# Performance work log

Hardware: AMD Instinct MI355X
Metric: run time of the kernel (lower is better)

## Reference

```python
import jax, jax.numpy as jnp
import numpy as np

B, C, H, W = 96, 5, 256, 256
T, V = 256, 256          # indices.shape[0], indices.shape[1]
HEADS, DHEAD = 2, 156
E = HEADS * DHEAD        # 312
EPS = 1e-5


def setup_inputs() -> dict:
    key = jax.random.key(0)
    ks = jax.random.split(key, 16)
    # indices: a permutation of the HxW grid so each pixel is gathered/scattered exactly once,
    # channel 2 is a float scale applied at scatter time.
    rng = np.random.RandomState(0)
    perm = rng.permutation(H * W).reshape(T, V)
    rows = (perm // W).astype(np.float32)
    cols = (perm % W).astype(np.float32)
    scale = rng.rand(T, V).astype(np.float32)
    indices = jnp.asarray(np.stack([rows, cols, scale], axis=-1))  # [T, V, 3]

    s = 0.02
    inp = {
        "sino": jax.random.normal(ks[0], (B, C, H, W), jnp.float32),
        "indices": indices,
        "We": jax.random.normal(ks[1], (C * V, E), jnp.float32) * s,
        "be": jnp.zeros((E,), jnp.float32),
        "pos": jax.random.normal(ks[2], (1, T, E), jnp.float32),
        "Wq": jax.random.normal(ks[3], (E, E), jnp.float32) * s,
        "Wk": jax.random.normal(ks[4], (E, E), jnp.float32) * s,
        "Wv": jax.random.normal(ks[5], (E, E), jnp.float32) * s,
        "W1": jax.random.normal(ks[6], (E, E), jnp.float32) * s,
        "b1": jnp.zeros((E,), jnp.float32),
        "W2": jax.random.normal(ks[7], (E, E), jnp.float32) * s,
        "b2": jnp.zeros((E,), jnp.float32),
        "W3": jax.random.normal(ks[8], (E, E), jnp.float32) * s,
        "b3": jnp.zeros((E,), jnp.float32),
        "g_att": jnp.ones((E,), jnp.float32),
        "beta_att": jnp.zeros((E,), jnp.float32),
        "g_mlp": jnp.ones((E,), jnp.float32),
        "beta_mlp": jnp.zeros((E,), jnp.float32),
        "Wu": jax.random.normal(ks[9], (E, V), jnp.float32) * s,
        "bu": jnp.zeros((V,), jnp.float32),
    }
    return inp


def _ln(y, g, b):
    m = jnp.mean(y, axis=-1, keepdims=True)
    v = jnp.var(y, axis=-1, keepdims=True)
    return (y - m) * jax.lax.rsqrt(v + EPS) * g + b


def reference(sino, indices, We, be, pos, Wq, Wk, Wv, W1, b1, W2, b2, W3, b3,
              g_att, beta_att, g_mlp, beta_mlp, Wu, bu):
    r = indices[:, :, 0].astype(jnp.int32)   # [T, V]
    c = indices[:, :, 1].astype(jnp.int32)   # [T, V]
    sc = indices[:, :, 2]                    # [T, V]

    # gather: sino[:, :, r, c] -> [B, C, T, V]
    x = sino[:, :, r, c]
    # 'bd c t v -> bd t (c v)'
    xt = jnp.transpose(x, (0, 2, 1, 3)).reshape(x.shape[0], T, C * V)
    Z = xt @ We + be + pos                   # [B, T, E]

    def split_heads(y):  # [B, T, E] -> [B, H, T, D]
        return y.reshape(y.shape[0], T, HEADS, DHEAD).transpose(0, 2, 1, 3)

    Q = split_heads(Z @ Wq)
    K = split_heads(Z @ Wk)
    Vh = split_heads(Z @ Wv)
    scores = jnp.einsum('bhnd,bhmd->bhnm', Q, K) * (DHEAD ** -0.5)
    att = jax.nn.softmax(scores, axis=-1)
    a = jnp.einsum('bhnm,bhmd->bhnd', att, Vh)          # [B, H, T, D]
    a = a.transpose(0, 2, 1, 3).reshape(Z.shape)        # 'b h n d -> b n (h d)'

    x1 = _ln(Z + a, g_att, beta_att)
    h = jax.nn.gelu(x1 @ W1 + b1, approximate=False)
    h = jax.nn.gelu(h @ W2 + b2, approximate=False)
    h = jax.nn.gelu(h @ W3 + b3, approximate=False)
    x2 = _ln(x1 + h, g_mlp, beta_mlp)

    out = (x2 @ Wu + bu)[:, None]                       # [B, 1, T, V]
    sino_out = sino[:, -1:, :, :]                       # [B, 1, H, W]
    out_full = jnp.zeros_like(sino_out).at[:, :, r, c].set(out * sc)
    return sino_out + out_full
```

## Files before the change

### kernel.cpp

```cpp
#include <hip/hip_runtime.h>
#include <math.h>

constexpr int B_  = 96;
constexpr int T_  = 256;
constexpr int V_  = 256;
constexpr int C_  = 5;
constexpr int H_  = 256;
constexpr int W_  = 256;
constexpr int NH_ = 2;
constexpr int DH_ = 156;
constexpr int E_  = 312;
constexpr int EP_ = 320;
constexpr int DHP_ = 160;
constexpr int CV_ = 1280;
constexpr int M_  = B_ * T_;

typedef short short8 __attribute__((ext_vector_type(8)));
typedef float f32x4 __attribute__((ext_vector_type(4)));

__device__ inline short f2bf(float f) {
    unsigned u = __builtin_bit_cast(unsigned, f);
    u = (u + 0x7fff + ((u >> 16) & 1)) >> 16;
    return (short)u;
}

__device__ inline void gld16(const void* g, void* l) {
    __builtin_amdgcn_global_load_lds(
        (const __attribute__((address_space(1))) unsigned*)g,
        (__attribute__((address_space(3))) unsigned*)l, 16, 0, 0);
}

__global__ __launch_bounds__(256)
void gather_kernel(const float* __restrict__ sino, const float* __restrict__ idx,
                   short* __restrict__ xt) {
    int bid = blockIdx.x;
    int xcd = bid & 7, slot = bid >> 3;
    int sub = slot & 15, pidx = slot >> 4;
    int plane = pidx * 8 + xcd;
    int b = plane / C_, ch = plane - b * C_;
    const float* sp = sino + ((size_t)b * C_ + ch) * (H_ * W_);
    int tid = threadIdx.x;
    #pragma unroll
    for (int tt = 0; tt < 16; ++tt) {
        int t = sub * 16 + tt;
        int tv = t * 256 + tid;
        int r  = (int)idx[(size_t)tv * 3 + 0];
        int cc = (int)idx[(size_t)tv * 3 + 1];
        xt[(((size_t)b * T_ + t) * C_ + ch) * V_ + tid] = f2bf(sp[r * W_ + cc]);
    }
}

__global__ __launch_bounds__(256)
void wconv_kernel(const float* __restrict__ Wsrc, short* __restrict__ Wt,
                  int Ks, int Ns, int KP, int NP) {
    int idx = blockIdx.x * 256 + threadIdx.x;
    if (idx >= NP * KP) return;
    int n = idx / KP, k = idx - n * KP;
    Wt[idx] = (n < Ns && k < Ks) ? f2bf(Wsrc[(size_t)k * Ns + n]) : (short)0;
}

__global__ __launch_bounds__(256)
void zero_kernel(float4* __restrict__ p, size_t n4) {
    size_t i = (size_t)blockIdx.x * 256 + threadIdx.x;
    size_t stride = (size_t)gridDim.x * 256;
    float4 z; z.x = z.y = z.z = z.w = 0.f;
    for (; i < n4; i += stride) p[i] = z;
}

#define EPI_EMBED    0
#define EPI_QK       1
#define EPI_VT       2
#define EPI_SCORE    3
#define EPI_AV       4
#define EPI_GELU_BF  5
#define EPI_GELU_F32 6
#define EPI_OUT      7

template <int EPI>
__global__ __launch_bounds__(128)
void mgemm(const short* __restrict__ Aall, const short* __restrict__ Ball,
           const float* __restrict__ bias, const float* __restrict__ pos,
           float* __restrict__ Of, short* __restrict__ Ob,
           int K, int strideA, int strideB) {
    __shared__ __align__(16) char smem[24576];
    const int tid = threadIdx.x;
    const int wv = tid >> 6, ln = tid & 63;
    const int lr = ln & 15, lq = ln >> 4;
    const int z = blockIdx.z;

    const short* A;
    const short* Bt;
    if (EPI == EPI_SCORE)      { A = Aall + (size_t)z * 256 * DHP_; Bt = Ball + (size_t)z * 256 * DHP_; }
    else if (EPI == EPI_AV)    { A = Aall + (size_t)z * 256 * 256;  Bt = Ball + (size_t)z * 192 * 256; }
    else                       { A = Aall; Bt = Ball; }

    const int rm0 = blockIdx.y * 128;
    const int n0  = blockIdx.x * 64;
    const char* Abase = (const char*)(A + (size_t)rm0 * strideA);
    const char* Bbase = (const char*)(Bt + (size_t)n0 * strideB);
    const size_t sA = (size_t)strideA * 2, sB = (size_t)strideB * 2;

    f32x4 acc[4][4];
    #pragma unroll
    for (int mi = 0; mi < 4; ++mi)
        #pragma unroll
        for (int ni = 0; ni < 4; ++ni) acc[mi][ni] = {0.f, 0.f, 0.f, 0.f};

    const int KT = K >> 5;

    auto stage = [&](int buf, int kt) {
        const char* ab = Abase + (size_t)kt * 64;
        char* la = smem + buf * 12288;
        #pragma unroll
        for (int c = 0; c < 4; ++c) {
            int p = wv * 4096 + c * 1024 + ln * 16;
            int r = p >> 6;
            int cc = (p & 63) ^ (((p >> 7) & 3) << 4);
            gld16(ab + (size_t)r * sA + cc, la + wv * 4096 + c * 1024);
        }
        const char* bb = Bbase + (size_t)kt * 64;
        char* lb = smem + buf * 12288 + 8192;
        #pragma unroll
        for (int c = 0; c < 2; ++c) {
            int p = wv * 2048 + c * 1024 + ln * 16;
            int r = p >> 6;
            int cc = (p & 63) ^ (((p >> 7) & 3) << 4);
            gld16(bb + (size_t)r * sB + cc, lb + wv * 2048 + c * 1024);
        }
    };

    stage(0, 0);
    for (int kt = 0; kt < KT; ++kt) {
        __syncthreads();
        if (kt + 1 < KT) stage((kt + 1) & 1, kt + 1);
        const char* la = smem + (kt & 1) * 12288;
        const char* lb = la + 8192;
        short8 af[4], bfv[4];
        #pragma unroll
        for (int mi = 0; mi < 4; ++mi) {
            int r = wv * 64 + mi * 16 + lr;
            af[mi] = *(const short8*)(la + r * 64 + ((lq * 16) ^ (((r >> 1) & 3) << 4)));
        }
        #pragma unroll
        for (int ni = 0; ni < 4; ++ni) {
            int n = ni * 16 + lr;
            bfv[ni] = *(const short8*)(lb + n * 64 + ((lq * 16) ^ (((n >> 1) & 3) << 4)));
        }
        #pragma unroll
        for (int mi = 0; mi < 4; ++mi)
            #pragma unroll
            for (int ni = 0; ni < 4; ++ni)
                acc[mi][ni] = __builtin_amdgcn_mfma_f32_16x16x32_bf16(
                    af[mi], bfv[ni], acc[mi][ni], 0, 0, 0);
    }

    #pragma unroll
    for (int mi = 0; mi < 4; ++mi) {
        #pragma unroll
        for (int i = 0; i < 4; ++i) {
            int gm = rm0 + wv * 64 + mi * 16 + lq * 4 + i;
            #pragma unroll
            for (int ni = 0; ni < 4; ++ni) {
                int gn = n0 + ni * 16 + lr;
                float v = acc[mi][ni][i];
                if (EPI == EPI_EMBED) {
                    if (gn < E_) v += bias[gn] + pos[(size_t)(gm & 255) * E_ + gn];
                    else v = 0.f;
                    Of[(size_t)gm * EP_ + gn] = v;
                    Ob[(size_t)gm * EP_ + gn] = f2bf(v);
                } else if (EPI == EPI_QK) {
                    if (gn < E_) {
                        int h = gn >= DH_;
                        int d = gn - h * DH_;
                        Ob[(((size_t)(gm >> 8) * NH_ + h) * 256 + (gm & 255)) * DHP_ + d] = f2bf(v);
                    }
                } else if (EPI == EPI_VT) {
                    if (gn < E_) {
                        int h = gn >= DH_;
                        int d = gn - h * DH_;
                        Ob[(((size_t)(gm >> 8) * NH_ + h) * 192 + d) * 256 + (gm & 255)] = f2bf(v);
                    }
                } else if (EPI == EPI_SCORE) {
                    Of[((size_t)z * 256 + gm) * 256 + gn] = v * 0.08006407690254357f;
                } else if (EPI == EPI_AV) {
                    if (gn < DH_) {
                        int b = z >> 1, h = z & 1;
                        Of[((size_t)b * 256 + gm) * EP_ + h * DH_ + gn] = v;
                    }
                } else if (EPI == EPI_GELU_BF) {
                    float bi = (gn < E_) ? bias[gn] : 0.f;
                    v += bi;
                    v = 0.5f * v * (1.f + erff(v * 0.70710678118654752f));
                    if (gn >= E_) v = 0.f;
                    Ob[(size_t)gm * EP_ + gn] = f2bf(v);
                } else if (EPI == EPI_GELU_F32) {
                    float bi = (gn < E_) ? bias[gn] : 0.f;
                    v += bi;
                    v = 0.5f * v * (1.f + erff(v * 0.70710678118654752f));
                    if (gn >= E_) v = 0.f;
                    Of[(size_t)gm * EP_ + gn] = v;
                } else if (EPI == EPI_OUT) {
                    v += bias[gn];
                    Of[(size_t)gm * 256 + gn] = v;
                }
            }
        }
    }
}

__global__ __launch_bounds__(256)
void softmax_bf(const float* __restrict__ S, short* __restrict__ P) {
    size_t row = blockIdx.x;
    int tid = threadIdx.x;
    const float* p = S + row * 256;
    __shared__ float red[256];
    float v = p[tid];
    red[tid] = v; __syncthreads();
    for (int off = 128; off > 0; off >>= 1) {
        if (tid < off) red[tid] = fmaxf(red[tid], red[tid + off]);
        __syncthreads();
    }
    float mx = red[0]; __syncthreads();
    float e = expf(v - mx);
    red[tid] = e; __syncthreads();
    for (int off = 128; off > 0; off >>= 1) {
        if (tid < off) red[tid] += red[tid + off];
        __syncthreads();
    }
    P[row * 256 + tid] = f2bf(e / red[0]);
}

template <bool DUAL>
__global__ __launch_bounds__(256)
void ln_kernel(const float* __restrict__ A, const float* __restrict__ Bi,
               const float* __restrict__ g, const float* __restrict__ beta,
               short* __restrict__ Outb, float* __restrict__ Outf) {
    int row = blockIdx.x;
    size_t base = (size_t)row * EP_;
    int tid = threadIdx.x;
    __shared__ float red[256];
    __shared__ float red2[256];

    float ya = A[base + tid] + Bi[base + tid];
    int t2 = tid + 256;
    float yb = (t2 < E_) ? A[base + t2] + Bi[base + t2] : 0.f;
    red[tid]  = ya + yb;
    red2[tid] = ya * ya + yb * yb;
    __syncthreads();
    for (int off = 128; off > 0; off >>= 1) {
        if (tid < off) { red[tid] += red[tid + off]; red2[tid] += red2[tid + off]; }
        __syncthreads();
    }
    float mean = red[0] / (float)E_;
    float var  = red2[0] / (float)E_ - mean * mean;
    float inv  = rsqrtf(var + 1e-5f);
    float oa = (ya - mean) * inv * g[tid] + beta[tid];
    Outb[base + tid] = f2bf(oa);
    if (DUAL) Outf[base + tid] = oa;
    if (t2 < E_) {
        float ob = (yb - mean) * inv * g[t2] + beta[t2];
        Outb[base + t2] = f2bf(ob);
        if (DUAL) Outf[base + t2] = ob;
    } else if (t2 < EP_) {
        Outb[base + t2] = 0;
        if (DUAL) Outf[base + t2] = 0.f;
    }
}

__global__ __launch_bounds__(256)
void scatter_kernel(const float* __restrict__ sino, const float* __restrict__ idx,
                    const float* __restrict__ outm, float* __restrict__ dout) {
    size_t i = (size_t)blockIdx.x * 256 + threadIdx.x;
    size_t total = (size_t)B_ * T_ * V_;
    if (i >= total) return;
    int tv = (int)(i % ((size_t)T_ * V_));
    int b  = (int)(i / ((size_t)T_ * V_));
    int r  = (int)idx[(size_t)tv * 3 + 0];
    int cc = (int)idx[(size_t)tv * 3 + 1];
    float sc = idx[(size_t)tv * 3 + 2];
    size_t pos = (size_t)r * W_ + cc;
    dout[(size_t)b * H_ * W_ + pos] =
        sino[((size_t)b * C_ + (C_ - 1)) * (size_t)H_ * W_ + pos] + outm[i] * sc;
}

extern "C" void kernel_launch(void* const* d_in, const int* in_sizes, int n_in,
                              void* d_out, int out_size, void* d_ws, size_t ws_size,
                              hipStream_t stream) {
    const float* sino     = (const float*)d_in[0];
    const float* idx      = (const float*)d_in[1];
    const float* We       = (const float*)d_in[2];
    const float* be       = (const float*)d_in[3];
    const float* pos      = (const float*)d_in[4];
    const float* Wq       = (const float*)d_in[5];
    const float* Wk       = (const float*)d_in[6];
    const float* Wv       = (const float*)d_in[7];
    const float* W1       = (const float*)d_in[8];
    const float* b1       = (const float*)d_in[9];
    const float* W2       = (const float*)d_in[10];
    const float* b2       = (const float*)d_in[11];
    const float* W3       = (const float*)d_in[12];
    const float* b3       = (const float*)d_in[13];
    const float* g_att    = (const float*)d_in[14];
    const float* beta_att = (const float*)d_in[15];
    const float* g_mlp    = (const float*)d_in[16];
    const float* beta_mlp = (const float*)d_in[17];
    const float* Wu       = (const float*)d_in[18];
    const float* bu       = (const float*)d_in[19];
    float* out = (float*)d_out;
    char* w = (char*)d_ws;

    const size_t oA = 0;
    const size_t oB = oA + 62914560;
    const size_t oC = oB + 31457280;
    const size_t oD = oC + 25165824;
    const size_t oE = oD + 15728640;
    const size_t oF = oE + 15728640;
    const size_t oG = oF + 31457280;
    const size_t oH = oG + 31457280;
    const size_t oW = oH + 25165824;

    short* xt_bf = (short*)(w + oA);
    float* Sf    = (float*)(w + oA);
    float* h3f   = (float*)(w + oA);
    float* Zf    = (float*)(w + oB);
    short* h1b   = (short*)(w + oB);
    short* Zb    = (short*)(w + oC);
    short* Pb    = (short*)(w + oC);
    short* Qh    = (short*)(w + oD);
    short* x1b   = (short*)(w + oD);
    short* Kh    = (short*)(w + oE);
    short* h2b   = (short*)(w + oE);
    short* Vt    = (short*)(w + oF);
    float* x1f   = (float*)(w + oF);
    float* abf   = (float*)(w + oG);
    short* x2b   = (short*)(w + oG);
    float* outm  = (float*)(w + oH);
    short* We_t  = (short*)(w + oW);
    short* Wq_t  = We_t + 409600;
    short* Wk_t  = Wq_t + 102400;
    short* Wv_t  = Wk_t + 102400;
    short* W1_t  = Wv_t + 102400;
    short* W2_t  = W1_t + 102400;
    short* W3_t  = W2_t + 102400;
    short* Wu_t  = W3_t + 102400;

    gather_kernel<<<dim3(7680), dim3(256), 0, stream>>>(sino, idx, xt_bf);

    wconv_kernel<<<dim3(1600), dim3(256), 0, stream>>>(We, We_t, 1280, E_, 1280, EP_);
    wconv_kernel<<<dim3(400), dim3(256), 0, stream>>>(Wq, Wq_t, E_, E_, EP_, EP_);
    wconv_kernel<<<dim3(400), dim3(256), 0, stream>>>(Wk, Wk_t, E_, E_, EP_, EP_);
    wconv_kernel<<<dim3(400), dim3(256), 0, stream>>>(Wv, Wv_t, E_, E_, EP_, EP_);
    wconv_kernel<<<dim3(400), dim3(256), 0, stream>>>(W1, W1_t, E_, E_, EP_, EP_);
    wconv_kernel<<<dim3(400), dim3(256), 0, stream>>>(W2, W2_t, E_, E_, EP_, EP_);
    wconv_kernel<<<dim3(400), dim3(256), 0, stream>>>(W3, W3_t, E_, E_, EP_, EP_);
    wconv_kernel<<<dim3(320), dim3(256), 0, stream>>>(Wu, Wu_t, E_, 256, EP_, 256);

    zero_kernel<<<dim3(4096), dim3(256), 0, stream>>>((float4*)(w + oD), 50331648 / 16);

    mgemm<EPI_EMBED><<<dim3(EP_ / 64, M_ / 128), dim3(128), 0, stream>>>(
        xt_bf, We_t, be, pos, Zf, Zb, CV_, CV_, CV_);

    mgemm<EPI_QK><<<dim3(EP_ / 64, M_ / 128), dim3(128), 0, stream>>>(
        Zb, Wq_t, nullptr, nullptr, nullptr, Qh, EP_, EP_, EP_);
    mgemm<EPI_QK><<<dim3(EP_ / 64, M_ / 128), dim3(128), 0, stream>>>(
        Zb, Wk_t, nullptr, nullptr, nullptr, Kh, EP_, EP_, EP_);
    mgemm<EPI_VT><<<dim3(EP_ / 64, M_ / 128), dim3(128), 0, stream>>>(
        Zb, Wv_t, nullptr, nullptr, nullptr, Vt, EP_, EP_, EP_);

    mgemm<EPI_SCORE><<<dim3(4, 2, B_ * NH_), dim3(128), 0, stream>>>(
        Qh, Kh, nullptr, nullptr, Sf, nullptr, DHP_, DHP_, DHP_);
    softmax_bf<<<dim3(B_ * NH_ * 256), dim3(256), 0, stream>>>(Sf, Pb);
    mgemm<EPI_AV><<<dim3(3, 2, B_ * NH_), dim3(128), 0, stream>>>(
        Pb, Vt, nullptr, nullptr, abf, nullptr, 256, 256, 256);

    ln_kernel<true><<<dim3(M_), dim3(256), 0, stream>>>(Zf, abf, g_att, beta_att, x1b, x1f);

    mgemm<EPI_GELU_BF><<<dim3(EP_ / 64, M_ / 128), dim3(128), 0, stream>>>(
        x1b, W1_t, b1, nullptr, nullptr, h1b, EP_, EP_, EP_);
    mgemm<EPI_GELU_BF><<<dim3(EP_ / 64, M_ / 128), dim3(128), 0, stream>>>(
        h1b, W2_t, b2, nullptr, nullptr, h2b, EP_, EP_, EP_);
    mgemm<EPI_GELU_F32><<<dim3(EP_ / 64, M_ / 128), dim3(128), 0, stream>>>(
        h2b, W3_t, b3, nullptr, h3f, nullptr, EP_, EP_, EP_);

    ln_kernel<false><<<dim3(M_), dim3(256), 0, stream>>>(x1f, h3f, g_mlp, beta_mlp, x2b, nullptr);

    mgemm<EPI_OUT><<<dim3(256 / 64, M_ / 128), dim3(128), 0, stream>>>(
        x2b, Wu_t, bu, nullptr, outm, nullptr, EP_, EP_, EP_);

    scatter_kernel<<<dim3((B_ * T_ * V_) / 256), dim3(256), 0, stream>>>(sino, idx, outm, out);
}
```

Measured before the change: 850.5 us.

## Fuse attention score GEMM with softmax and drop workspace zeroing

Result: faster. 796.9 us (-6.3%).

```diff
diff --git a/kernel.cpp b/kernel.cpp
--- a/kernel.cpp
+++ b/kernel.cpp
@@ -40,14 +40,22 @@
     int b = plane / C_, ch = plane - b * C_;
     const float* sp = sino + ((size_t)b * C_ + ch) * (H_ * W_);
     int tid = threadIdx.x;
+
+    int addr[16];
     #pragma unroll
     for (int tt = 0; tt < 16; ++tt) {
-        int t = sub * 16 + tt;
-        int tv = t * 256 + tid;
+        int tv = (sub * 16 + tt) * 256 + tid;
         int r  = (int)idx[(size_t)tv * 3 + 0];
         int cc = (int)idx[(size_t)tv * 3 + 1];
-        xt[(((size_t)b * T_ + t) * C_ + ch) * V_ + tid] = f2bf(sp[r * W_ + cc]);
-    }
+        addr[tt] = r * W_ + cc;
+    }
+    float pix[16];
+    #pragma unroll
+    for (int tt = 0; tt < 16; ++tt) pix[tt] = sp[addr[tt]];
+    size_t dbase = (((size_t)b * T_ + sub * 16) * C_ + ch) * V_ + tid;
+    #pragma unroll
+    for (int tt = 0; tt < 16; ++tt)
+        xt[dbase + (size_t)tt * (C_ * V_)] = f2bf(pix[tt]);
 }
 
 __global__ __launch_bounds__(256)
@@ -59,18 +67,9 @@
     Wt[idx] = (n < Ns && k < Ks) ? f2bf(Wsrc[(size_t)k * Ns + n]) : (short)0;
 }
 
-__global__ __launch_bounds__(256)
-void zero_kernel(float4* __restrict__ p, size_t n4) {
-    size_t i = (size_t)blockIdx.x * 256 + threadIdx.x;
-    size_t stride = (size_t)gridDim.x * 256;
-    float4 z; z.x = z.y = z.z = z.w = 0.f;
-    for (; i < n4; i += stride) p[i] = z;
-}
-
 #define EPI_EMBED    0
 #define EPI_QK       1
 #define EPI_VT       2
-#define EPI_SCORE    3
 #define EPI_AV       4
 #define EPI_GELU_BF  5
 #define EPI_GELU_F32 6
@@ -90,9 +89,8 @@
 
     const short* A;
     const short* Bt;
-    if (EPI == EPI_SCORE)      { A = Aall + (size_t)z * 256 * DHP_; Bt = Ball + (size_t)z * 256 * DHP_; }
-    else if (EPI == EPI_AV)    { A = Aall + (size_t)z * 256 * 256;  Bt = Ball + (size_t)z * 192 * 256; }
-    else                       { A = Aall; Bt = Ball; }
+    if (EPI == EPI_AV) { A = Aall + (size_t)z * 256 * 256;  Bt = Ball + (size_t)z * 192 * 256; }
+    else               { A = Aall; Bt = Ball; }
 
     const int rm0 = blockIdx.y * 128;
     const int n0  = blockIdx.x * 64;
@@ -173,6 +171,11 @@
                         int h = gn >= DH_;
                         int d = gn - h * DH_;
                         Ob[(((size_t)(gm >> 8) * NH_ + h) * 256 + (gm & 255)) * DHP_ + d] = f2bf(v);
+                    } else {
+                        int pi = gn - E_;
+                        int h = pi >> 2;
+                        int d = DH_ + (pi & 3);
+                        Ob[(((size_t)(gm >> 8) * NH_ + h) * 256 + (gm & 255)) * DHP_ + d] = (short)0;
                     }
                 } else if (EPI == EPI_VT) {
                     if (gn < E_) {
@@ -180,8 +183,6 @@
                         int d = gn - h * DH_;
                         Ob[(((size_t)(gm >> 8) * NH_ + h) * 192 + d) * 256 + (gm & 255)] = f2bf(v);
                     }
-                } else if (EPI == EPI_SCORE) {
-                    Of[((size_t)z * 256 + gm) * 256 + gn] = v * 0.08006407690254357f;
                 } else if (EPI == EPI_AV) {
                     if (gn < DH_) {
                         int b = z >> 1, h = z & 1;
@@ -209,25 +210,126 @@
 }
 
 __global__ __launch_bounds__(256)
-void softmax_bf(const float* __restrict__ S, short* __restrict__ P) {
-    size_t row = blockIdx.x;
-    int tid = threadIdx.x;
-    const float* p = S + row * 256;
-    __shared__ float red[256];
-    float v = p[tid];
-    red[tid] = v; __syncthreads();
-    for (int off = 128; off > 0; off >>= 1) {
-        if (tid < off) red[tid] = fmaxf(red[tid], red[tid + off]);
+void score_softmax_kernel(const short* __restrict__ Qh, const short* __restrict__ Kh,
+                          short* __restrict__ P) {
+    __shared__ __align__(16) char smem[40960];
+    __shared__ float redm[4][64];
+    __shared__ float reds[4][64];
+    const int tid = threadIdx.x;
+    const int wv = tid >> 6, ln = tid & 63;
+    const int lr = ln & 15, lq = ln >> 4;
+    const int z = blockIdx.y;
+    const int q0 = blockIdx.x * 64;
+
+    const size_t sA = DHP_ * 2;
+    const char* Qbase = (const char*)(Qh + (size_t)z * 256 * DHP_) + (size_t)q0 * sA;
+    const char* Kbase = (const char*)(Kh + (size_t)z * 256 * DHP_);
+
+    f32x4 acc[4][4];
+    #pragma unroll
+    for (int mi = 0; mi < 4; ++mi)
+        #pragma unroll
+        for (int ni = 0; ni < 4; ++ni) acc[mi][ni] = {0.f, 0.f, 0.f, 0.f};
+
+    auto stage = [&](int buf, int kt) {
+        char* la = smem + buf * 20480;
+        {
+            int p = tid * 16;
+            int r = p >> 6;
+            int cc = (p & 63) ^ (((p >> 7) & 3) << 4);
+            gld16(Qbase + (size_t)kt * 64 + (size_t)r * sA + cc, la + p);
+        }
+        char* lb = la + 4096;
+        #pragma unroll
+        for (int c = 0; c < 4; ++c) {
+            int p = c * 4096 + tid * 16;
+            int r = p >> 6;
+            int cc = (p & 63) ^ (((p >> 7) & 3) << 4);
+            gld16(Kbase + (size_t)kt * 64 + (size_t)r * sA + cc, lb + p);
+        }
+    };
+
+    stage(0, 0);
+    for (int kt = 0; kt < 5; ++kt) {
         __syncthreads();
-    }
-    float mx = red[0]; __syncthreads();
-    float e = expf(v - mx);
-    red[tid] = e; __syncthreads();
-    for (int off = 128; off > 0; off >>= 1) {
-        if (tid < off) red[tid] += red[tid + off];
-        __syncthreads();
-    }
-    P[row * 256 + tid] = f2bf(e / red[0]);
+        if (kt + 1 < 5) stage((kt + 1) & 1, kt + 1);
+        const char* la = smem + (kt & 1) * 20480;
+        const char* lb = la + 4096;
+        short8 af[4], bfv[4];
+        #pragma unroll
+        for (int mi = 0; mi < 4; ++mi) {
+            int r = mi * 16 + lr;
+            af[mi] = *(const short8*)(la + r * 64 + ((lq * 16) ^ (((r >> 1) & 3) << 4)));
+        }
+        #pragma unroll
+        for (int ni = 0; ni < 4; ++ni) {
+            int n = wv * 64 + ni * 16 + lr;
+            bfv[ni] = *(const short8*)(lb + n * 64 + ((lq * 16) ^ (((n >> 1) & 3) << 4)));
+        }
+        #pragma unroll
+        for (int mi = 0; mi < 4; ++mi)
+            #pragma unroll
+            for (int ni = 0; ni < 4; ++ni)
+                acc[mi][ni] = __builtin_amdgcn_mfma_f32_16x16x32_bf16(
+                    af[mi], bfv[ni], acc[mi][ni], 0, 0, 0);
+    }
+
+    const float scale = 0.08006407690254357f;
+    #pragma unroll
+    for (int mi = 0; mi < 4; ++mi)
+        #pragma unroll
+        for (int ni = 0; ni < 4; ++ni)
+            #pragma unroll
+            for (int i = 0; i < 4; ++i) acc[mi][ni][i] *= scale;
+
+    #pragma unroll
+    for (int mi = 0; mi < 4; ++mi) {
+        #pragma unroll
+        for (int i = 0; i < 4; ++i) {
+            float m = fmaxf(fmaxf(acc[mi][0][i], acc[mi][1][i]),
+                            fmaxf(acc[mi][2][i], acc[mi][3][i]));
+            #pragma unroll
+            for (int off = 1; off < 16; off <<= 1) m = fmaxf(m, __shfl_xor(m, off));
+            if (lr == 0) redm[wv][mi * 16 + lq * 4 + i] = m;
+        }
+    }
+    __syncthreads();
+    #pragma unroll
+    for (int mi = 0; mi < 4; ++mi) {
+        #pragma unroll
+        for (int i = 0; i < 4; ++i) {
+            int rl = mi * 16 + lq * 4 + i;
+            float m = fmaxf(fmaxf(redm[0][rl], redm[1][rl]),
+                            fmaxf(redm[2][rl], redm[3][rl]));
+            float s = 0.f;
+            #pragma unroll
+            for (int ni = 0; ni < 4; ++ni) {
+                float e = expf(acc[mi][ni][i] - m);
+                acc[mi][ni][i] = e;
+                s += e;
+            }
+            #pragma unroll
+            for (int off = 1; off < 16; off <<= 1) s += __shfl_xor(s, off);
+            if (lr == 0) reds[wv][rl] = s;
+        }
+    }
+    __syncthreads();
+
+    short* Pz = P + (size_t)z * 256 * 256;
+    #pragma unroll
+    for (int mi = 0; mi < 4; ++mi) {
+        #pragma unroll
+        for (int i = 0; i < 4; ++i) {
+            int rl = mi * 16 + lq * 4 + i;
+            float inv = 1.f / (reds[0][rl] + reds[1][rl] + reds[2][rl] + reds[3][rl]);
+            int gm = q0 + rl;
+            #pragma unroll
+            for (int ni = 0; ni < 4; ++ni) {
+                int gn = wv * 64 + ni * 16 + lr;
+                Pz[(size_t)gm * 256 + gn] = f2bf(acc[mi][ni][i] * inv);
+            }
+        }
+    }
 }
 
 template <bool DUAL>
@@ -320,7 +422,6 @@
     const size_t oW = oH + 25165824;
 
     short* xt_bf = (short*)(w + oA);
-    float* Sf    = (float*)(w + oA);
     float* h3f   = (float*)(w + oA);
     float* Zf    = (float*)(w + oB);
     short* h1b   = (short*)(w + oB);
@@ -355,8 +456,6 @@
     wconv_kernel<<<dim3(400), dim3(256), 0, stream>>>(W3, W3_t, E_, E_, EP_, EP_);
     wconv_kernel<<<dim3(320), dim3(256), 0, stream>>>(Wu, Wu_t, E_, 256, EP_, 256);
 
-    zero_kernel<<<dim3(4096), dim3(256), 0, stream>>>((float4*)(w + oD), 50331648 / 16);
-
     mgemm<EPI_EMBED><<<dim3(EP_ / 64, M_ / 128), dim3(128), 0, stream>>>(
         xt_bf, We_t, be, pos, Zf, Zb, CV_, CV_, CV_);
 
@@ -367,9 +466,7 @@
     mgemm<EPI_VT><<<dim3(EP_ / 64, M_ / 128), dim3(128), 0, stream>>>(
         Zb, Wv_t, nullptr, nullptr, nullptr, Vt, EP_, EP_, EP_);
 
-    mgemm<EPI_SCORE><<<dim3(4, 2, B_ * NH_), dim3(128), 0, stream>>>(
-        Qh, Kh, nullptr, nullptr, Sf, nullptr, DHP_, DHP_, DHP_);
-    softmax_bf<<<dim3(B_ * NH_ * 256), dim3(256), 0, stream>>>(Sf, Pb);
+    score_softmax_kernel<<<dim3(4, 192), dim3(256), 0, stream>>>(Qh, Kh, Pb);
     mgemm<EPI_AV><<<dim3(3, 2, B_ * NH_), dim3(128), 0, stream>>>(
         Pb, Vt, nullptr, nullptr, abf, nullptr, 256, 256, 256);
 
```
